# Optimization experiments

Measured on AMD Instinct MI355X. Metric: run time of the kernel, lower is better.

Reference implementation:

```python
import jax, jax.numpy as jnp
import numpy as np

D = 256          # B == num_experts == hidden_dim == input_dim (required by the module's broadcasting)
NUM_HEADS = 4
LN_EPS = 1e-5


def _layer_norm(x, g, b):
    mu = jnp.mean(x, axis=-1, keepdims=True)
    var = jnp.mean(jnp.square(x - mu), axis=-1, keepdims=True)
    return (x - mu) * jax.lax.rsqrt(var + LN_EPS) * g + b


def setup_inputs() -> dict:
    key = jax.random.key(0)
    ks = jax.random.split(key, 12)
    B = E = H = IN = D
    s = 0.02
    return {
        "x": jax.random.normal(ks[0], (B, IN), jnp.float32),
        "task_embedding": jax.random.normal(ks[1], (B, H), jnp.float32),
        # stacked per-expert params: Linear(IN,H) -> LayerNorm(H) -> ReLU -> Linear(H,H)
        "W1": jax.random.normal(ks[2], (E, H, IN), jnp.float32) * s,
        "b1": jnp.zeros((E, H), jnp.float32),
        "ln1_g": jnp.ones((E, H), jnp.float32),
        "ln1_b": jnp.zeros((E, H), jnp.float32),
        "W2": jax.random.normal(ks[3], (E, H, H), jnp.float32) * s,
        "b2": jnp.zeros((E, H), jnp.float32),
        # MultiheadAttention in-projection (packed q,k,v). v/out_proj are dead code
        # in this forward (attn_output is discarded) but v slice kept for faithful shapes.
        "in_proj_w": jax.random.normal(ks[4], (3 * H, H), jnp.float32) * s,
        "in_proj_b": jnp.zeros((3 * H,), jnp.float32),
        # combine: Linear(H,H) -> LayerNorm(H) -> ReLU
        "cw": jax.random.normal(ks[5], (H, H), jnp.float32) * s,
        "cb": jnp.zeros((H,), jnp.float32),
        "cg": jnp.ones((H,), jnp.float32),
        "cbeta": jnp.zeros((H,), jnp.float32),
    }


def reference(x, task_embedding, W1, b1, ln1_g, ln1_b, W2, b2,
              in_proj_w, in_proj_b, cw, cb, cg, cbeta):
    B, H = x.shape
    hd = H // NUM_HEADS

    # ---- all experts on the same input (batched over expert axis) ----
    h = jnp.einsum('bi,eoi->beo', x, W1) + b1          # [B,E,H]
    h = _layer_norm(h, ln1_g, ln1_b)
    h = jax.nn.relu(h)
    eo = jnp.einsum('beh,eoh->beo', h, W2) + b2        # [B,E,H] expert_outputs

    # ---- attention gate (only attn_weights are used downstream) ----
    Wq, Wk = in_proj_w[:H], in_proj_w[H:2 * H]
    bq, bk = in_proj_b[:H], in_proj_b[H:2 * H]
    q = (task_embedding @ Wq.T + bq).reshape(B, NUM_HEADS, hd) / jnp.sqrt(jnp.float32(hd))
    k = (jnp.einsum('beh,oh->beo', eo, Wk) + bk).reshape(B, -1, NUM_HEADS, hd)
    scores = jnp.einsum('bnd,bend->bne', q, k)          # [B, heads, E]
    attn = jax.nn.softmax(scores, axis=-1)
    weights = jnp.mean(attn, axis=1)                    # [B, E] (avg over heads)

    # ---- faithful torch broadcasting of [B,E,H] * [1,B,E] (requires B==E==H) ----
    # combined[b,h] = sum_e eo[b,e,h] * weights[e,h]
    combined = jnp.einsum('beh,eh->bh', eo, weights)

    out = jax.nn.relu(_layer_norm(combined @ cw.T + cb, cg, cbeta))
    return out, weights[:, None, :], eo
```

## Files before the change

### kernel.cpp

```cpp
#include <hip/hip_runtime.h>

typedef _Float16 f16_t;
typedef f16_t f16x8 __attribute__((ext_vector_type(8)));
typedef float f32x4 __attribute__((ext_vector_type(4)));

#define MFMA16(a,b,c) __builtin_amdgcn_mfma_f32_16x16x32_f16(a,b,c,0,0,0)
#define VM0 asm volatile("s_waitcnt vmcnt(0)" ::: "memory")
#define VM2 asm volatile("s_waitcnt vmcnt(2)" ::: "memory")

__device__ __forceinline__ void cp16(const void* g, void* l){
  __builtin_amdgcn_global_load_lds(
      (const __attribute__((address_space(1))) void*)g,
      (__attribute__((address_space(3))) void*)l, 16, 0, 0);
}

__device__ __forceinline__ f16x8 cvt8h(float4 a, float4 b){
  f16x8 r;
  r[0]=(f16_t)a.x; r[1]=(f16_t)a.y; r[2]=(f16_t)a.z; r[3]=(f16_t)a.w;
  r[4]=(f16_t)b.x; r[5]=(f16_t)b.y; r[6]=(f16_t)b.z; r[7]=(f16_t)b.w;
  return r;
}

template<int NT>
__device__ __forceinline__ void stage_f16(const float* __restrict__ src,
                                          char* dst, int rows, int tid){
  const int nchunk = rows * 32;
  const float4* s4 = reinterpret_cast<const float4*>(src);
  for (int cid = tid; cid < nchunk; cid += NT){
    int r = cid >> 5, c = cid & 31;
    *reinterpret_cast<f16x8*>(dst + r*512 + ((c ^ (r&7))<<4)) = cvt8h(s4[cid*2], s4[cid*2+1]);
  }
}

__device__ __forceinline__ f16x8 ldsA(const char* buf, int row, int c16){
  return *reinterpret_cast<const f16x8*>(buf + row*512 + ((c16 ^ (row&7))<<4));
}

__device__ __forceinline__ void issue_tile(const f16_t* wsrc_lane, int kb, char* wt, int lane){
  const f16_t* s = wsrc_lane + kb*32;
  char* d = wt + (kb&1)*2048 + lane*16;
  cp16(s, d);
  cp16(s + 16*256, d + 1024);
}

__device__ __forceinline__ void gemm_pipe(f32x4 acc[4][2], const char* bufA,
    const f16_t* wsrc_lane, char* wt, int lane, int lo16, int hi4){
  #pragma unroll
  for (int kb = 0; kb < 8; ++kb){
    if (kb < 7) { VM2; } else { VM0; }
    const char* ws = wt + (kb&1)*2048 + lane*16;
    f16x8 bf0 = *reinterpret_cast<const f16x8*>(ws);
    f16x8 bf1 = *reinterpret_cast<const f16x8*>(ws + 1024);
    #pragma unroll
    for (int mb = 0; mb < 4; ++mb){
      f16x8 af = ldsA(bufA, mb*16 + lo16, kb*4 + hi4);
      acc[mb][0] = MFMA16(af, bf0, acc[mb][0]);
      acc[mb][1] = MFMA16(af, bf1, acc[mb][1]);
    }
    __builtin_amdgcn_sched_barrier(0);
    if (kb + 2 < 8) issue_tile(wsrc_lane, kb + 2, wt, lane);
  }
}

__device__ __forceinline__ void gemm_w32(f32x4 acc[4][2], const char* bufA,
    const float* __restrict__ W, int n0, int lo16, int hi4){
  #pragma unroll
  for (int kb = 0; kb < 8; ++kb){
    f16x8 bf[2];
    #pragma unroll
    for (int nb = 0; nb < 2; ++nb){
      const float4* p = reinterpret_cast<const float4*>(W + ((n0 + nb*16 + lo16)<<8) + kb*32 + hi4*8);
      bf[nb] = cvt8h(p[0], p[1]);
    }
    #pragma unroll
    for (int mb = 0; mb < 4; ++mb){
      f16x8 af = ldsA(bufA, mb*16 + lo16, kb*4 + hi4);
      acc[mb][0] = MFMA16(af, bf[0], acc[mb][0]);
      acc[mb][1] = MFMA16(af, bf[1], acc[mb][1]);
    }
  }
}

__global__ __launch_bounds__(256)
void k0_cvt(const float* __restrict__ W1, const float* __restrict__ W2,
            const float* __restrict__ Wk, f16_t* __restrict__ w1h,
            f16_t* __restrict__ w2h, f16_t* __restrict__ wkh)
{
  const long long NG1 = 2097152, NG2 = 4194304, NGT = 4202496;
  for (long long gidx = (long long)blockIdx.x*256 + threadIdx.x; gidx < NGT;
       gidx += (long long)gridDim.x*256){
    const float4* s; f16_t* d; long long off;
    if (gidx < NG1){ s = (const float4*)W1; d = w1h; off = gidx; }
    else if (gidx < NG2){ s = (const float4*)W2; d = w2h; off = gidx - NG1; }
    else { s = (const float4*)Wk; d = wkh; off = gidx - NG2; }
    *reinterpret_cast<f16x8*>(d + off*8) = cvt8h(s[off*2], s[off*2+1]);
  }
}

template<int W16>
__global__ __launch_bounds__(512, 4)
void k2_fused(const float* __restrict__ x, const void* __restrict__ W1v,
              const float* __restrict__ b1, const float* __restrict__ g1,
              const float* __restrict__ bb1, const void* __restrict__ W2v,
              const float* __restrict__ b2, const void* __restrict__ Wkv,
              const float* __restrict__ ipb, const float* __restrict__ q,
              float* __restrict__ eo_out, float* __restrict__ scores)
{
  __shared__ __align__(16) char lds[70144];
  char* bufA = lds;
  float* red = (float*)(lds + 32768);
  float* st  = (float*)(lds + 36864);
  char* wpipe = lds + 37376;

  const int l = blockIdx.x;
  const int e    = (l & 7) * 32 + (l >> 5);
  const int b0   = ((l >> 3) & 3) * 64;
  const int tid = threadIdx.x;
  const int lane = tid & 63, wid = tid >> 6;
  const int lo16 = lane & 15, hi4 = lane >> 4;
  const int n0 = wid * 32;
  char* wt = wpipe + wid*4096;

  const int pl = (n0 + (lane & 15))*256 + (lane >> 4)*8;
  const f16_t* src1 = nullptr; const f16_t* src2 = nullptr; const f16_t* srcK = nullptr;
  if (W16){
    src1 = (const f16_t*)W1v + e*65536 + pl;
    src2 = (const f16_t*)W2v + e*65536 + pl;
    srcK = (const f16_t*)Wkv + pl;
    issue_tile(src1, 0, wt, lane);
    issue_tile(src1, 1, wt, lane);
  }

  stage_f16<512>(x + b0*256, bufA, 64, tid);
  __syncthreads();

  f32x4 acc[4][2];
  #pragma unroll
  for (int mb=0;mb<4;++mb){
    #pragma unroll
    for (int nb=0;nb<2;++nb) acc[mb][nb] = (f32x4)0.0f;
  }

  if (W16) gemm_pipe(acc, bufA, src1, wt, lane, lo16, hi4);
  else     gemm_w32(acc, bufA, (const float*)W1v + e*65536, n0, lo16, hi4);

  if (W16){
    issue_tile(src2, 0, wt, lane);
    issue_tile(src2, 1, wt, lane);
  }

  float b1v[2], g1v[2], bbv[2];
  #pragma unroll
  for (int nb=0;nb<2;++nb){
    int c = n0 + nb*16 + lo16;
    b1v[nb] = b1[e*256 + c];
    g1v[nb] = g1[e*256 + c];
    bbv[nb] = bb1[e*256 + c];
  }
  #pragma unroll
  for (int mb=0;mb<4;++mb){
    #pragma unroll
    for (int nb=0;nb<2;++nb){
      #pragma unroll
      for (int r=0;r<4;++r) acc[mb][nb][r] += b1v[nb];
    }
  }

  #pragma unroll
  for (int mb=0;mb<4;++mb){
    #pragma unroll
    for (int r=0;r<4;++r){
      float s=0.f, ss=0.f;
      #pragma unroll
      for (int nb=0;nb<2;++nb){ float v = acc[mb][nb][r]; s += v; ss += v*v; }
      #pragma unroll
      for (int m=1;m<16;m<<=1){ s += __shfl_xor(s, m, 64); ss += __shfl_xor(ss, m, 64); }
      if (lo16 == 0){
        int row = mb*16 + hi4*4 + r;
        red[row*16 + wid]     = s;
        red[row*16 + 8 + wid] = ss;
      }
    }
  }
  __syncthreads();
  if (tid < 64){
    float s  = 0.f, ss = 0.f;
    #pragma unroll
    for (int i=0;i<8;++i){ s += red[tid*16 + i]; ss += red[tid*16 + 8 + i]; }
    float mu = s * (1.f/256.f);
    float var = ss * (1.f/256.f) - mu*mu;
    st[tid*2]   = mu;
    st[tid*2+1] = rsqrtf(var + 1e-5f);
  }
  __syncthreads();

  #pragma unroll
  for (int mb=0;mb<4;++mb){
    #pragma unroll
    for (int r=0;r<4;++r){
      int row = mb*16 + hi4*4 + r;
      float mu = st[row*2], rs = st[row*2+1];
      #pragma unroll
      for (int nb=0;nb<2;++nb){
        int c = n0 + nb*16 + lo16;
        float v = (acc[mb][nb][r] - mu) * rs * g1v[nb] + bbv[nb];
        v = fmaxf(v, 0.f);
        int off = row*512 + (((c>>3) ^ (row&7))<<4) + (c&7)*2;
        *reinterpret_cast<f16_t*>(bufA + off) = (f16_t)v;
      }
    }
  }
  __syncthreads();

  #pragma unroll
  for (int mb=0;mb<4;++mb){
    #pragma unroll
    for (int nb=0;nb<2;++nb) acc[mb][nb] = (f32x4)0.0f;
  }
  if (W16) gemm_pipe(acc, bufA, src2, wt, lane, lo16, hi4);
  else     gemm_w32(acc, bufA, (const float*)W2v + e*65536, n0, lo16, hi4);

  float b2v[2];
  #pragma unroll
  for (int nb=0;nb<2;++nb) b2v[nb] = b2[e*256 + n0 + nb*16 + lo16];

  __syncthreads();

  if (W16){
    issue_tile(srcK, 0, wt, lane);
    issue_tile(srcK, 1, wt, lane);
  }

  #pragma unroll
  for (int mb=0;mb<4;++mb){
    #pragma unroll
    for (int r=0;r<4;++r){
      int row = mb*16 + hi4*4 + r;
      int b = b0 + row;
      #pragma unroll
      for (int nb=0;nb<2;++nb){
        int c = n0 + nb*16 + lo16;
        float v = acc[mb][nb][r] + b2v[nb];
        eo_out[(b*256 + e)*256 + c] = v;
        int off = row*512 + (((c>>3) ^ (row&7))<<4) + (c&7)*2;
        *reinterpret_cast<f16_t*>(bufA + off) = (f16_t)v;
      }
    }
  }
  __syncthreads();

  #pragma unroll
  for (int mb=0;mb<4;++mb){
    #pragma unroll
    for (int nb=0;nb<2;++nb) acc[mb][nb] = (f32x4)0.0f;
  }
  if (W16) gemm_pipe(acc, bufA, srcK, wt, lane, lo16, hi4);
  else     gemm_w32(acc, bufA, (const float*)Wkv, n0, lo16, hi4);

  float bkv[2];
  #pragma unroll
  for (int nb=0;nb<2;++nb) bkv[nb] = ipb[256 + n0 + nb*16 + lo16];

  #pragma unroll
  for (int mb=0;mb<4;++mb){
    #pragma unroll
    for (int r=0;r<4;++r){
      int row = mb*16 + hi4*4 + r;
      int b = b0 + row;
      float p = 0.f;
      #pragma unroll
      for (int nb=0;nb<2;++nb){
        int c = n0 + nb*16 + lo16;
        p += q[b*256 + c] * (acc[mb][nb][r] + bkv[nb]);
      }
      #pragma unroll
      for (int m=1;m<16;m<<=1) p += __shfl_xor(p, m, 64);
      if (lo16 == 0) red[row*16 + wid] = p;
    }
  }
  __syncthreads();
  if (tid < 256){
    int row = tid >> 2, hd = tid & 3;
    float sc = red[row*16 + hd*2] + red[row*16 + hd*2 + 1];
    scores[((b0 + row)*4 + hd)*256 + e] = sc;
  }
}

__global__ __launch_bounds__(512, 4)
void k_mini(const float* __restrict__ A, const float* __restrict__ W,
            const float* __restrict__ bias, float scale, int do_ln,
            const float* __restrict__ g, const float* __restrict__ bb,
            int do_relu, float* __restrict__ out)
{
  __shared__ __align__(16) char lds[18688];
  char* bufA = lds;
  float* red = (float*)(lds + 16384);
  float* st  = (float*)(lds + 18432);

  const int b0 = blockIdx.x * 32;
  const int tid = threadIdx.x;
  const int lane = tid & 63, wid = tid >> 6;
  const int lo16 = lane & 15, hi4 = lane >> 4;
  const int n0 = wid * 32;

  stage_f16<512>(A + b0*256, bufA, 32, tid);
  __syncthreads();

  f32x4 acc[2][2];
  #pragma unroll
  for (int mb=0;mb<2;++mb){
    #pragma unroll
    for (int nb=0;nb<2;++nb) acc[mb][nb] = (f32x4)0.0f;
  }
  #pragma unroll
  for (int kb = 0; kb < 8; ++kb){
    f16x8 bf[2];
    #pragma unroll
    for (int nb = 0; nb < 2; ++nb){
      const float4* p = reinterpret_cast<const float4*>(W + ((n0 + nb*16 + lo16)<<8) + kb*32 + hi4*8);
      bf[nb] = cvt8h(p[0], p[1]);
    }
    #pragma unroll
    for (int mb = 0; mb < 2; ++mb){
      f16x8 af = ldsA(bufA, mb*16 + lo16, kb*4 + hi4);
      acc[mb][0] = MFMA16(af, bf[0], acc[mb][0]);
      acc[mb][1] = MFMA16(af, bf[1], acc[mb][1]);
    }
  }

  float bv[2], gv[2], bbv[2];
  #pragma unroll
  for (int nb=0;nb<2;++nb){
    int c = n0 + nb*16 + lo16;
    bv[nb]  = bias[c];
    gv[nb]  = do_ln ? g[c]  : 1.f;
    bbv[nb] = do_ln ? bb[c] : 0.f;
  }
  #pragma unroll
  for (int mb=0;mb<2;++mb){
    #pragma unroll
    for (int nb=0;nb<2;++nb){
      #pragma unroll
      for (int r=0;r<4;++r) acc[mb][nb][r] = (acc[mb][nb][r] + bv[nb]) * scale;
    }
  }

  if (do_ln){
    #pragma unroll
    for (int mb=0;mb<2;++mb){
      #pragma unroll
      for (int r=0;r<4;++r){
        float s=0.f, ss=0.f;
        #pragma unroll
        for (int nb=0;nb<2;++nb){ float v = acc[mb][nb][r]; s += v; ss += v*v; }
        #pragma unroll
        for (int m=1;m<16;m<<=1){ s += __shfl_xor(s, m, 64); ss += __shfl_xor(ss, m, 64); }
        if (lo16 == 0){
          int row = mb*16 + hi4*4 + r;
          red[row*16 + wid]     = s;
          red[row*16 + 8 + wid] = ss;
        }
      }
    }
    __syncthreads();
    if (tid < 32){
      float s = 0.f, ss = 0.f;
      #pragma unroll
      for (int i=0;i<8;++i){ s += red[tid*16 + i]; ss += red[tid*16 + 8 + i]; }
      float mu = s * (1.f/256.f);
      float var = ss * (1.f/256.f) - mu*mu;
      st[tid*2]   = mu;
      st[tid*2+1] = rsqrtf(var + 1e-5f);
    }
    __syncthreads();
  }

  #pragma unroll
  for (int mb=0;mb<2;++mb){
    #pragma unroll
    for (int r=0;r<4;++r){
      int row = mb*16 + hi4*4 + r;
      float mu = 0.f, rs = 1.f;
      if (do_ln){ mu = st[row*2]; rs = st[row*2+1]; }
      #pragma unroll
      for (int nb=0;nb<2;++nb){
        int c = n0 + nb*16 + lo16;
        float v = acc[mb][nb][r];
        if (do_ln) v = (v - mu) * rs * gv[nb] + bbv[nb];
        if (do_relu) v = fmaxf(v, 0.f);
        out[(b0 + row)*256 + c] = v;
      }
    }
  }
}

__global__ __launch_bounds__(256)
void k3_softmax(const float* __restrict__ scores, float* __restrict__ wts)
{
  const int b = blockIdx.x, t = threadIdx.x;
  const int wid = t >> 6, lane = t & 63;
  __shared__ float r4[4];
  float sc[4];
  #pragma unroll
  for (int n=0;n<4;++n) sc[n] = scores[(b*4 + n)*256 + t];
  float wsum = 0.f;
  for (int n=0;n<4;++n){
    float m = sc[n];
    #pragma unroll
    for (int k=1;k<64;k<<=1) m = fmaxf(m, __shfl_xor(m, k, 64));
    if (lane == 0) r4[wid] = m;
    __syncthreads();
    m = fmaxf(fmaxf(r4[0], r4[1]), fmaxf(r4[2], r4[3]));
    __syncthreads();
    float ex = __expf(sc[n] - m);
    float s = ex;
    #pragma unroll
    for (int k=1;k<64;k<<=1) s += __shfl_xor(s, k, 64);
    if (lane == 0) r4[wid] = s;
    __syncthreads();
    s = r4[0] + r4[1] + r4[2] + r4[3];
    __syncthreads();
    wsum += ex / s;
  }
  wts[b*256 + t] = wsum * 0.25f;
}

__global__ __launch_bounds__(1024)
void k4a_combined(const float* __restrict__ eo, const float* __restrict__ wts,
                  float* __restrict__ cmb)
{
  __shared__ float part[1024];
  const int b = blockIdx.x, t = threadIdx.x;
  const int c = t >> 8, h = t & 255;
  const float* p = eo + b*65536 + h;
  float s = 0.f;
  #pragma unroll 8
  for (int i = 0; i < 64; ++i){
    int e2 = c*64 + i;
    s += p[e2*256] * wts[e2*256 + h];
  }
  part[t] = s;
  __syncthreads();
  if (t < 256) cmb[b*256 + t] = part[t] + part[t+256] + part[t+512] + part[t+768];
}

extern "C" void kernel_launch(void* const* d_in, const int* in_sizes, int n_in,
                              void* d_out, int out_size, void* d_ws, size_t ws_size,
                              hipStream_t stream)
{
  const float* x    = (const float*)d_in[0];
  const float* te   = (const float*)d_in[1];
  const float* W1   = (const float*)d_in[2];
  const float* b1   = (const float*)d_in[3];
  const float* g1   = (const float*)d_in[4];
  const float* bb1  = (const float*)d_in[5];
  const float* W2   = (const float*)d_in[6];
  const float* b2   = (const float*)d_in[7];
  const float* ipw  = (const float*)d_in[8];
  const float* ipb  = (const float*)d_in[9];
  const float* cw   = (const float*)d_in[10];
  const float* cb   = (const float*)d_in[11];
  const float* cg   = (const float*)d_in[12];
  const float* cbt  = (const float*)d_in[13];

  float* out    = (float*)d_out;
  float* wts    = out + 65536;
  float* eo     = out + 131072;

  const size_t F16_BYTES = 2ull*(16777216ull*2 + 65536);
  const size_t NEED = F16_BYTES + 4ull*(65536 + 262144 + 65536);
  const bool f16w = ws_size >= NEED;

  f16_t* w1h = (f16_t*)d_ws;
  f16_t* w2h = w1h + 16777216;
  f16_t* wkh = w2h + 16777216;
  float* fbase = f16w ? (float*)((char*)d_ws + F16_BYTES) : (float*)d_ws;
  float* q      = fbase;
  float* scores = q + 65536;
  float* cmb    = scores + 262144;

  k_mini<<<8, 512, 0, stream>>>(te, ipw, ipb, 0.125f, 0, nullptr, nullptr, 0, q);

  if (f16w){
    k0_cvt<<<2048, 256, 0, stream>>>(W1, W2, ipw + 65536, w1h, w2h, wkh);
    k2_fused<1><<<1024, 512, 0, stream>>>(x, w1h, b1, g1, bb1, w2h, b2,
                                          wkh, ipb, q, eo, scores);
  } else {
    k2_fused<0><<<1024, 512, 0, stream>>>(x, W1, b1, g1, bb1, W2, b2,
                                          ipw + 65536, ipb, q, eo, scores);
  }

  k3_softmax<<<256, 256, 0, stream>>>(scores, wts);
  k4a_combined<<<256, 1024, 0, stream>>>(eo, wts, cmb);
  k_mini<<<8, 512, 0, stream>>>(cmb, cw, cb, 1.0f, 1, cg, cbt, 1, out);
}
```

Measured before the change: 149.5 us.

## Fold key projection into query to drop third GEMM from fused expert kernel

Uses the identity q·(eo·Wk^T + bk) = eo·(q·Wk per head) + q·bk. A new small kernel precomputes q·Wk per batch row and head as f16 plus the bias term, so the fused expert kernel replaces its third 64x256x256 GEMM, with its LDS staging and barriers, by a per-element dot product against the precomputed vector. Wk no longer needs f16 conversion, and workspace buffers are aliased more tightly. Also raises wave priority around the MFMA block in the GEMM pipeline; the extra kernel launch and f16 rounding of the folded vector are the costs.

Measured after the change: 153.4 us. +2.7%, slower.

```diff
diff --git a/kernel.cpp b/kernel.cpp
--- a/kernel.cpp
+++ b/kernel.cpp
@@ -2,6 +2,7 @@
 
 typedef _Float16 f16_t;
 typedef f16_t f16x8 __attribute__((ext_vector_type(8)));
+typedef f16_t f16x4 __attribute__((ext_vector_type(4)));
 typedef float f32x4 __attribute__((ext_vector_type(4)));
 
 #define MFMA16(a,b,c) __builtin_amdgcn_mfma_f32_16x16x32_f16(a,b,c,0,0,0)
@@ -51,12 +52,14 @@
     const char* ws = wt + (kb&1)*2048 + lane*16;
     f16x8 bf0 = *reinterpret_cast<const f16x8*>(ws);
     f16x8 bf1 = *reinterpret_cast<const f16x8*>(ws + 1024);
+    __builtin_amdgcn_s_setprio(1);
     #pragma unroll
     for (int mb = 0; mb < 4; ++mb){
       f16x8 af = ldsA(bufA, mb*16 + lo16, kb*4 + hi4);
       acc[mb][0] = MFMA16(af, bf0, acc[mb][0]);
       acc[mb][1] = MFMA16(af, bf1, acc[mb][1]);
     }
+    __builtin_amdgcn_s_setprio(0);
     __builtin_amdgcn_sched_barrier(0);
     if (kb + 2 < 8) issue_tile(wsrc_lane, kb + 2, wt, lane);
   }
@@ -83,17 +86,42 @@
 
 __global__ __launch_bounds__(256)
 void k0_cvt(const float* __restrict__ W1, const float* __restrict__ W2,
-            const float* __restrict__ Wk, f16_t* __restrict__ w1h,
-            f16_t* __restrict__ w2h, f16_t* __restrict__ wkh)
-{
-  const long long NG1 = 2097152, NG2 = 4194304, NGT = 4202496;
+            f16_t* __restrict__ w1h, f16_t* __restrict__ w2h)
+{
+  const long long NG1 = 2097152, NGT = 4194304;
   for (long long gidx = (long long)blockIdx.x*256 + threadIdx.x; gidx < NGT;
        gidx += (long long)gridDim.x*256){
     const float4* s; f16_t* d; long long off;
     if (gidx < NG1){ s = (const float4*)W1; d = w1h; off = gidx; }
-    else if (gidx < NG2){ s = (const float4*)W2; d = w2h; off = gidx - NG1; }
-    else { s = (const float4*)Wk; d = wkh; off = gidx - NG2; }
+    else { s = (const float4*)W2; d = w2h; off = gidx - NG1; }
     *reinterpret_cast<f16x8*>(d + off*8) = cvt8h(s[off*2], s[off*2+1]);
+  }
+}
+
+__global__ __launch_bounds__(256)
+void kqwk(const float* __restrict__ q, const float* __restrict__ Wk,
+          const float* __restrict__ ipb, f16_t* __restrict__ qWkT,
+          float* __restrict__ qbk)
+{
+  __shared__ float qrow[256];
+  const int b = blockIdx.x, t = threadIdx.x;
+  qrow[t] = q[b*256 + t];
+  __syncthreads();
+  float s0=0.f, s1=0.f, s2=0.f, s3=0.f;
+  #pragma unroll 8
+  for (int d = 0; d < 64; ++d){
+    s0 += qrow[d]       * Wk[ d       *256 + t];
+    s1 += qrow[64 + d]  * Wk[(64 + d) *256 + t];
+    s2 += qrow[128 + d] * Wk[(128 + d)*256 + t];
+    s3 += qrow[192 + d] * Wk[(192 + d)*256 + t];
+  }
+  f16x4 o; o[0]=(f16_t)s0; o[1]=(f16_t)s1; o[2]=(f16_t)s2; o[3]=(f16_t)s3;
+  *reinterpret_cast<f16x4*>(qWkT + (b*256 + t)*4) = o;
+  if (t < 4){
+    float sb = 0.f;
+    #pragma unroll 8
+    for (int d = 0; d < 64; ++d) sb += qrow[t*64 + d] * ipb[256 + t*64 + d];
+    qbk[b*4 + t] = sb;
   }
 }
 
@@ -102,15 +130,15 @@
 void k2_fused(const float* __restrict__ x, const void* __restrict__ W1v,
               const float* __restrict__ b1, const float* __restrict__ g1,
               const float* __restrict__ bb1, const void* __restrict__ W2v,
-              const float* __restrict__ b2, const void* __restrict__ Wkv,
-              const float* __restrict__ ipb, const float* __restrict__ q,
+              const float* __restrict__ b2, const f16_t* __restrict__ qWkT,
+              const float* __restrict__ qbk,
               float* __restrict__ eo_out, float* __restrict__ scores)
 {
-  __shared__ __align__(16) char lds[70144];
+  __shared__ __align__(16) char lds[74240];
   char* bufA = lds;
   float* red = (float*)(lds + 32768);
-  float* st  = (float*)(lds + 36864);
-  char* wpipe = lds + 37376;
+  float* st  = (float*)(lds + 40960);
+  char* wpipe = lds + 41472;
 
   const int l = blockIdx.x;
   const int e    = (l & 7) * 32 + (l >> 5);
@@ -122,11 +150,10 @@
   char* wt = wpipe + wid*4096;
 
   const int pl = (n0 + (lane & 15))*256 + (lane >> 4)*8;
-  const f16_t* src1 = nullptr; const f16_t* src2 = nullptr; const f16_t* srcK = nullptr;
+  const f16_t* src1 = nullptr; const f16_t* src2 = nullptr;
   if (W16){
     src1 = (const f16_t*)W1v + e*65536 + pl;
     src2 = (const f16_t*)W2v + e*65536 + pl;
-    srcK = (const f16_t*)Wkv + pl;
     issue_tile(src1, 0, wt, lane);
     issue_tile(src1, 1, wt, lane);
   }
@@ -149,13 +176,14 @@
     issue_tile(src2, 1, wt, lane);
   }
 
-  float b1v[2], g1v[2], bbv[2];
+  float b1v[2], g1v[2], bbv[2], b2v[2];
   #pragma unroll
   for (int nb=0;nb<2;++nb){
     int c = n0 + nb*16 + lo16;
     b1v[nb] = b1[e*256 + c];
     g1v[nb] = g1[e*256 + c];
     bbv[nb] = bb1[e*256 + c];
+    b2v[nb] = b2[e*256 + c];
   }
   #pragma unroll
   for (int mb=0;mb<4;++mb){
@@ -220,69 +248,44 @@
   if (W16) gemm_pipe(acc, bufA, src2, wt, lane, lo16, hi4);
   else     gemm_w32(acc, bufA, (const float*)W2v + e*65536, n0, lo16, hi4);
 
-  float b2v[2];
-  #pragma unroll
-  for (int nb=0;nb<2;++nb) b2v[nb] = b2[e*256 + n0 + nb*16 + lo16];
-
-  __syncthreads();
-
-  if (W16){
-    issue_tile(srcK, 0, wt, lane);
-    issue_tile(srcK, 1, wt, lane);
-  }
-
   #pragma unroll
   for (int mb=0;mb<4;++mb){
     #pragma unroll
     for (int r=0;r<4;++r){
       int row = mb*16 + hi4*4 + r;
       int b = b0 + row;
+      float p0=0.f, p1=0.f, p2=0.f, p3=0.f;
       #pragma unroll
       for (int nb=0;nb<2;++nb){
         int c = n0 + nb*16 + lo16;
         float v = acc[mb][nb][r] + b2v[nb];
         eo_out[(b*256 + e)*256 + c] = v;
-        int off = row*512 + (((c>>3) ^ (row&7))<<4) + (c&7)*2;
-        *reinterpret_cast<f16_t*>(bufA + off) = (f16_t)v;
-      }
-    }
-  }
-  __syncthreads();
-
-  #pragma unroll
-  for (int mb=0;mb<4;++mb){
-    #pragma unroll
-    for (int nb=0;nb<2;++nb) acc[mb][nb] = (f32x4)0.0f;
-  }
-  if (W16) gemm_pipe(acc, bufA, srcK, wt, lane, lo16, hi4);
-  else     gemm_w32(acc, bufA, (const float*)Wkv, n0, lo16, hi4);
-
-  float bkv[2];
-  #pragma unroll
-  for (int nb=0;nb<2;++nb) bkv[nb] = ipb[256 + n0 + nb*16 + lo16];
-
-  #pragma unroll
-  for (int mb=0;mb<4;++mb){
-    #pragma unroll
-    for (int r=0;r<4;++r){
-      int row = mb*16 + hi4*4 + r;
-      int b = b0 + row;
-      float p = 0.f;
-      #pragma unroll
-      for (int nb=0;nb<2;++nb){
-        int c = n0 + nb*16 + lo16;
-        p += q[b*256 + c] * (acc[mb][nb][r] + bkv[nb]);
-      }
-      #pragma unroll
-      for (int m=1;m<16;m<<=1) p += __shfl_xor(p, m, 64);
-      if (lo16 == 0) red[row*16 + wid] = p;
+        f16x4 qk = *reinterpret_cast<const f16x4*>(qWkT + (b*256 + c)*4);
+        p0 += v * (float)qk[0];
+        p1 += v * (float)qk[1];
+        p2 += v * (float)qk[2];
+        p3 += v * (float)qk[3];
+      }
+      #pragma unroll
+      for (int m=1;m<16;m<<=1){
+        p0 += __shfl_xor(p0, m, 64); p1 += __shfl_xor(p1, m, 64);
+        p2 += __shfl_xor(p2, m, 64); p3 += __shfl_xor(p3, m, 64);
+      }
+      if (lo16 == 0){
+        red[row*32 + wid*4 + 0] = p0;
+        red[row*32 + wid*4 + 1] = p1;
+        red[row*32 + wid*4 + 2] = p2;
+        red[row*32 + wid*4 + 3] = p3;
+      }
     }
   }
   __syncthreads();
   if (tid < 256){
-    int row = tid >> 2, hd = tid & 3;
-    float sc = red[row*16 + hd*2] + red[row*16 + hd*2 + 1];
-    scores[((b0 + row)*4 + hd)*256 + e] = sc;
+    int row = tid >> 2, n = tid & 3;
+    float sc = 0.f;
+    #pragma unroll
+    for (int w=0;w<8;++w) sc += red[row*32 + w*4 + n];
+    scores[((b0 + row)*4 + n)*256 + e] = sc + qbk[(b0 + row)*4 + n];
   }
 }
 
@@ -467,27 +470,30 @@
   float* wts    = out + 65536;
   float* eo     = out + 131072;
 
-  const size_t F16_BYTES = 2ull*(16777216ull*2 + 65536);
-  const size_t NEED = F16_BYTES + 4ull*(65536 + 262144 + 65536);
+  const size_t F16_BYTES = 2ull * 16777216ull * 2;
+  const size_t NEED = F16_BYTES + 1048576 + 524288 + 4096;
   const bool f16w = ws_size >= NEED;
 
   f16_t* w1h = (f16_t*)d_ws;
   f16_t* w2h = w1h + 16777216;
-  f16_t* wkh = w2h + 16777216;
-  float* fbase = f16w ? (float*)((char*)d_ws + F16_BYTES) : (float*)d_ws;
-  float* q      = fbase;
-  float* scores = q + 65536;
-  float* cmb    = scores + 262144;
+  char* tail = f16w ? ((char*)d_ws + F16_BYTES) : (char*)d_ws;
+  float* regA  = (float*)tail;
+  f16_t* qwkt  = (f16_t*)(tail + 1048576);
+  float* qbk   = (float*)(tail + 1048576 + 524288);
+  float* q      = regA;
+  float* scores = regA;
+  float* cmb    = regA;
 
   k_mini<<<8, 512, 0, stream>>>(te, ipw, ipb, 0.125f, 0, nullptr, nullptr, 0, q);
+  kqwk<<<256, 256, 0, stream>>>(q, ipw + 65536, ipb, qwkt, qbk);
 
   if (f16w){
-    k0_cvt<<<2048, 256, 0, stream>>>(W1, W2, ipw + 65536, w1h, w2h, wkh);
+    k0_cvt<<<2048, 256, 0, stream>>>(W1, W2, w1h, w2h);
     k2_fused<1><<<1024, 512, 0, stream>>>(x, w1h, b1, g1, bb1, w2h, b2,
-                                          wkh, ipb, q, eo, scores);
+                                          qwkt, qbk, eo, scores);
   } else {
     k2_fused<0><<<1024, 512, 0, stream>>>(x, W1, b1, g1, bb1, W2, b2,
-                                          ipw + 65536, ipb, q, eo, scores);
+                                          qwkt, qbk, eo, scores);
   }
 
   k3_softmax<<<256, 256, 0, stream>>>(scores, wts);
```

## Fuse combine GEMM and layernorm into combined kernel; remap weight tile lanes

Applied to the files above, without the earlier changes.

The weighted expert sum, the final Linear, LayerNorm and ReLU now run in one kernel per batch row, using scalar FP32 dot products from LDS. This removes a kernel launch and the workspace round trip of the combined vector. In exchange, the small MFMA-based k_mini pass is replaced by scalar code. Separately, the async weight-tile load mapping in k2_fused changes so each group of four lanes fetches one contiguous 64-byte row. The LDS read offsets are adjusted to match, aiming at better global load coalescing.

New measurement: 141.7 us. 5.2% less time.

```diff
diff --git a/kernel.cpp b/kernel.cpp
--- a/kernel.cpp
+++ b/kernel.cpp
@@ -48,7 +48,7 @@
   #pragma unroll
   for (int kb = 0; kb < 8; ++kb){
     if (kb < 7) { VM2; } else { VM0; }
-    const char* ws = wt + (kb&1)*2048 + lane*16;
+    const char* ws = wt + (kb&1)*2048 + lo16*64 + hi4*16;
     f16x8 bf0 = *reinterpret_cast<const f16x8*>(ws);
     f16x8 bf1 = *reinterpret_cast<const f16x8*>(ws + 1024);
     #pragma unroll
@@ -121,7 +121,7 @@
   const int n0 = wid * 32;
   char* wt = wpipe + wid*4096;
 
-  const int pl = (n0 + (lane & 15))*256 + (lane >> 4)*8;
+  const int pl = (n0 + (lane >> 2))*256 + (lane & 3)*8;
   const f16_t* src1 = nullptr; const f16_t* src2 = nullptr; const f16_t* srcK = nullptr;
   if (W16){
     src1 = (const f16_t*)W1v + e*65536 + pl;
@@ -288,14 +288,11 @@
 
 __global__ __launch_bounds__(512, 4)
 void k_mini(const float* __restrict__ A, const float* __restrict__ W,
-            const float* __restrict__ bias, float scale, int do_ln,
-            const float* __restrict__ g, const float* __restrict__ bb,
-            int do_relu, float* __restrict__ out)
-{
-  __shared__ __align__(16) char lds[18688];
+            const float* __restrict__ bias, float scale,
+            float* __restrict__ out)
+{
+  __shared__ __align__(16) char lds[16384];
   char* bufA = lds;
-  float* red = (float*)(lds + 16384);
-  float* st  = (float*)(lds + 18432);
 
   const int b0 = blockIdx.x * 32;
   const int tid = threadIdx.x;
@@ -328,67 +325,19 @@
     }
   }
 
-  float bv[2], gv[2], bbv[2];
-  #pragma unroll
-  for (int nb=0;nb<2;++nb){
-    int c = n0 + nb*16 + lo16;
-    bv[nb]  = bias[c];
-    gv[nb]  = do_ln ? g[c]  : 1.f;
-    bbv[nb] = do_ln ? bb[c] : 0.f;
-  }
-  #pragma unroll
-  for (int mb=0;mb<2;++mb){
-    #pragma unroll
-    for (int nb=0;nb<2;++nb){
-      #pragma unroll
-      for (int r=0;r<4;++r) acc[mb][nb][r] = (acc[mb][nb][r] + bv[nb]) * scale;
-    }
-  }
-
-  if (do_ln){
-    #pragma unroll
-    for (int mb=0;mb<2;++mb){
-      #pragma unroll
-      for (int r=0;r<4;++r){
-        float s=0.f, ss=0.f;
-        #pragma unroll
-        for (int nb=0;nb<2;++nb){ float v = acc[mb][nb][r]; s += v; ss += v*v; }
-        #pragma unroll
-        for (int m=1;m<16;m<<=1){ s += __shfl_xor(s, m, 64); ss += __shfl_xor(ss, m, 64); }
-        if (lo16 == 0){
-          int row = mb*16 + hi4*4 + r;
-          red[row*16 + wid]     = s;
-          red[row*16 + 8 + wid] = ss;
-        }
-      }
-    }
-    __syncthreads();
-    if (tid < 32){
-      float s = 0.f, ss = 0.f;
-      #pragma unroll
-      for (int i=0;i<8;++i){ s += red[tid*16 + i]; ss += red[tid*16 + 8 + i]; }
-      float mu = s * (1.f/256.f);
-      float var = ss * (1.f/256.f) - mu*mu;
-      st[tid*2]   = mu;
-      st[tid*2+1] = rsqrtf(var + 1e-5f);
-    }
-    __syncthreads();
-  }
+  float bv[2];
+  #pragma unroll
+  for (int nb=0;nb<2;++nb) bv[nb] = bias[n0 + nb*16 + lo16];
 
   #pragma unroll
   for (int mb=0;mb<2;++mb){
     #pragma unroll
     for (int r=0;r<4;++r){
       int row = mb*16 + hi4*4 + r;
-      float mu = 0.f, rs = 1.f;
-      if (do_ln){ mu = st[row*2]; rs = st[row*2+1]; }
       #pragma unroll
       for (int nb=0;nb<2;++nb){
         int c = n0 + nb*16 + lo16;
-        float v = acc[mb][nb][r];
-        if (do_ln) v = (v - mu) * rs * gv[nb] + bbv[nb];
-        if (do_relu) v = fmaxf(v, 0.f);
-        out[(b0 + row)*256 + c] = v;
+        out[(b0 + row)*256 + c] = (acc[mb][nb][r] + bv[nb]) * scale;
       }
     }
   }
@@ -426,22 +375,65 @@
 }
 
 __global__ __launch_bounds__(1024)
-void k4a_combined(const float* __restrict__ eo, const float* __restrict__ wts,
-                  float* __restrict__ cmb)
+void kB_out(const float* __restrict__ eo, const float* __restrict__ wts,
+            const float* __restrict__ cw, const float* __restrict__ cb,
+            const float* __restrict__ cg, const float* __restrict__ cbt,
+            float* __restrict__ out)
 {
   __shared__ float part[1024];
+  __shared__ float cmb_l[256];
+  __shared__ float vl[256];
+  __shared__ float st2[2];
   const int b = blockIdx.x, t = threadIdx.x;
   const int c = t >> 8, h = t & 255;
-  const float* p = eo + b*65536 + h;
-  float s = 0.f;
-  #pragma unroll 8
-  for (int i = 0; i < 64; ++i){
-    int e2 = c*64 + i;
-    s += p[e2*256] * wts[e2*256 + h];
-  }
-  part[t] = s;
-  __syncthreads();
-  if (t < 256) cmb[b*256 + t] = part[t] + part[t+256] + part[t+512] + part[t+768];
+
+  {
+    const float* p = eo + b*65536 + h;
+    float s = 0.f;
+    #pragma unroll 8
+    for (int i = 0; i < 64; ++i){
+      int e2 = c*64 + i;
+      s += p[e2*256] * wts[e2*256 + h];
+    }
+    part[t] = s;
+  }
+  __syncthreads();
+  if (t < 256) cmb_l[t] = part[t] + part[t+256] + part[t+512] + part[t+768];
+  __syncthreads();
+
+  {
+    const float* cwr = cw + h*256 + c*64;
+    float y = 0.f;
+    #pragma unroll 8
+    for (int k = 0; k < 64; ++k) y += cmb_l[c*64 + k] * cwr[k];
+    part[t] = y;
+  }
+  __syncthreads();
+  if (t < 256) vl[t] = part[t] + part[t+256] + part[t+512] + part[t+768] + cb[t];
+  __syncthreads();
+
+  if (t < 64){
+    float s = 0.f, ss = 0.f;
+    #pragma unroll
+    for (int i = 0; i < 4; ++i){
+      float v = vl[t*4 + i];
+      s += v; ss += v*v;
+    }
+    #pragma unroll
+    for (int m=1;m<64;m<<=1){ s += __shfl_xor(s, m, 64); ss += __shfl_xor(ss, m, 64); }
+    if (t == 0){
+      float mu = s * (1.f/256.f);
+      float var = ss * (1.f/256.f) - mu*mu;
+      st2[0] = mu;
+      st2[1] = rsqrtf(var + 1e-5f);
+    }
+  }
+  __syncthreads();
+
+  if (t < 256){
+    float v = (vl[t] - st2[0]) * st2[1] * cg[t] + cbt[t];
+    out[b*256 + t] = fmaxf(v, 0.f);
+  }
 }
 
 extern "C" void kernel_launch(void* const* d_in, const int* in_sizes, int n_in,
@@ -468,7 +460,7 @@
   float* eo     = out + 131072;
 
   const size_t F16_BYTES = 2ull*(16777216ull*2 + 65536);
-  const size_t NEED = F16_BYTES + 4ull*(65536 + 262144 + 65536);
+  const size_t NEED = F16_BYTES + 4ull*65536 + 4ull*262144;
   const bool f16w = ws_size >= NEED;
 
   f16_t* w1h = (f16_t*)d_ws;
@@ -477,9 +469,8 @@
   float* fbase = f16w ? (float*)((char*)d_ws + F16_BYTES) : (float*)d_ws;
   float* q      = fbase;
   float* scores = q + 65536;
-  float* cmb    = scores + 262144;
-
-  k_mini<<<8, 512, 0, stream>>>(te, ipw, ipb, 0.125f, 0, nullptr, nullptr, 0, q);
+
+  k_mini<<<8, 512, 0, stream>>>(te, ipw, ipb, 0.125f, q);
 
   if (f16w){
     k0_cvt<<<2048, 256, 0, stream>>>(W1, W2, ipw + 65536, w1h, w2h, wkh);
@@ -491,6 +482,5 @@
   }
 
   k3_softmax<<<256, 256, 0, stream>>>(scores, wts);
-  k4a_combined<<<256, 1024, 0, stream>>>(eo, wts, cmb);
-  k_mini<<<8, 512, 0, stream>>>(cmb, cw, cb, 1.0f, 1, cg, cbt, 1, out);
-}
+  kB_out<<<256, 1024, 0, stream>>>(eo, wts, cw, cb, cg, cbt, out);
+}
```
